# Optimization experiments

Hardware: AMD Instinct MI355X
Metric: run time of the kernel (lower is better)

Reference implementation:

```python
import jax, jax.numpy as jnp
import numpy as np

B, N, HID, NHEADS, VOCAB = 8, 2048, 768, 4, 15
ALPHA = 0.2  # LeakyReLU negative slope
NEG = -9e15  # matches -9000000000000000.0 mask constant


def setup_inputs() -> dict:
    key = jax.random.key(0)
    ks = jax.random.split(key, 7)
    node_feats = jax.random.randint(ks[0], (B, N), 0, VOCAB, dtype=jnp.int32)
    adjs = jax.random.randint(ks[1], (B, N, N), 0, 2, dtype=jnp.int32)
    embed_table = jax.random.normal(ks[2], (VOCAB, HID), dtype=jnp.float32)
    W_heads = jax.random.normal(ks[3], (NHEADS, HID, HID), dtype=jnp.float32) * 0.05
    a_heads = jax.random.normal(ks[4], (NHEADS, 2 * HID, 1), dtype=jnp.float32) * 0.05
    W_out = jax.random.normal(ks[5], (NHEADS * HID, HID), dtype=jnp.float32) * 0.05
    a_out = jax.random.normal(ks[6], (2 * HID, 1), dtype=jnp.float32) * 0.05
    return {"node_feats": node_feats, "adjs": adjs, "embed_table": embed_table,
            "W_heads": W_heads, "a_heads": a_heads, "W_out": W_out, "a_out": a_out}


def gat_layer(h, adj, W, a, concat):
    # h: (B,N,Fin), adj: (B,N,N), W: (Fin,Fout), a: (2*Fout,1)
    Fout = W.shape[1]
    Wh = jnp.matmul(h, W)                      # (B,N,Fout)
    Wh1 = jnp.matmul(Wh, a[:Fout])             # (B,N,1)
    Wh2 = jnp.matmul(Wh, a[Fout:])             # (B,N,1)
    e = Wh1 + jnp.swapaxes(Wh2, 1, 2)          # (B,N,N)
    e = jax.nn.leaky_relu(e, negative_slope=ALPHA)
    e = jnp.where(adj > 0, e, NEG)
    att = jax.nn.softmax(e, axis=-1)           # (B,N,N)
    h_prime = jnp.matmul(att, Wh)              # (B,N,Fout)
    return jax.nn.elu(h_prime) if concat else h_prime


def reference(node_feats, adjs, embed_table, W_heads, a_heads, W_out, a_out):
    x = embed_table[node_feats]                # (B,N,HID)  (shape_enc treated as identity)
    # multi-head GAT, heads vmapped then concatenated along feature dim
    heads = jax.vmap(lambda W, a: gat_layer(x, adjs, W, a, concat=True))(W_heads, a_heads)
    x = jnp.concatenate(jnp.moveaxis(heads, 0, -2).reshape(B, N, 1, NHEADS * HID).squeeze(2)[None], axis=0)[0] if False else jnp.transpose(heads, (1, 2, 0, 3)).reshape(B, N, NHEADS * HID)
    x = jax.nn.elu(gat_layer(x, adjs, W_out, a_out, concat=False))  # (B,N,HID)
    # pooling_forward with all-ones mask -> masked mean over node dim
    sum_emb = jnp.sum(x, axis=1)               # (B,HID)
    denom = jnp.maximum(jnp.full_like(sum_emb, float(N)), 1e-9)
    return sum_emb / denom                     # (B,HID)
```

## Files before the change

### kernel.cpp

```cpp
#include <hip/hip_runtime.h>
#include <math.h>

#define BB 8
#define NN 2048
#define HID 768
#define NHEADS 4
#define VOCAB 15
#define ALPHA 0.2f
#define NEGV -9e15f
#define MTOT (BB * NN)

using short4v = __attribute__((ext_vector_type(4))) short;
using short8v = __attribute__((ext_vector_type(8))) short;
using f32x4 = __attribute__((ext_vector_type(4))) float;

__device__ __forceinline__ short f2bf(float f) {
  union { float f; unsigned u; } x;
  x.f = f;
  unsigned r = x.u + 0x7fffu + ((x.u >> 16) & 1u);
  return (short)(r >> 16);
}

__device__ __forceinline__ void cp16(const void* g, void* l) {
  __builtin_amdgcn_global_load_lds(
      (const __attribute__((address_space(1))) unsigned int*)g,
      (__attribute__((address_space(3))) unsigned int*)l, 16, 0, 0);
}

__device__ __forceinline__ unsigned long long nibcompress(unsigned long long x) {
  x = (x | (x >> 4)) & 0x00FF00FF00FF00FFull;
  x = (x | (x >> 8)) & 0x0000FFFF0000FFFFull;
  x = (x | (x >> 16)) & 0x00000000FFFFFFFFull;
  return x;
}

#define MEMFENCE asm volatile("" ::: "memory")
#define SBAR()                         \
  do {                                 \
    MEMFENCE;                          \
    __builtin_amdgcn_s_barrier();      \
    MEMFENCE;                          \
  } while (0)

#define PACK_B 32768
#define ZERO_B 308
#define NFM_B 64
#define TRAN_B 2304
#define TW_B 192
__global__ __launch_bounds__(256) void setup_kernel(
    const int* __restrict__ adj, unsigned long long* __restrict__ packed,
    float* __restrict__ zbase, const int* __restrict__ nf,
    unsigned long long* __restrict__ nfm, const float* __restrict__ W_out,
    short* __restrict__ Wt_o, const float* __restrict__ table,
    const float* __restrict__ W_heads, float* __restrict__ TWp) {
  const int bid = blockIdx.x;
  const int tid = threadIdx.x;
  if (bid < PACK_B) {
    __shared__ unsigned long long nibq[32];
    long base = (long)bid * 1024;
    int4 a = *(const int4*)(adj + base + tid * 4);
    unsigned nib = (a.x > 0 ? 1u : 0u) | (a.y > 0 ? 2u : 0u) |
                   (a.z > 0 ? 4u : 0u) | (a.w > 0 ? 8u : 0u);
    ((unsigned char*)nibq)[tid] = (unsigned char)nib;
    __syncthreads();
    if (tid < 16) {
      unsigned long long lo = nibcompress(nibq[2 * tid]);
      unsigned long long hi = nibcompress(nibq[2 * tid + 1]);
      packed[(base >> 6) + tid] = lo | (hi << 32);
    }
  } else if (bid < PACK_B + ZERO_B) {
    zbase[(bid - PACK_B) * 256 + tid] = 0.f;
  } else if (bid < PACK_B + ZERO_B + NFM_B) {
    int r = bid - PACK_B - ZERO_B;
    int b = r >> 3, c = r & 7;
    int w = tid >> 6;
    int j = c * 256 + tid;
    int nfv = nf[b * NN + j];
#pragma unroll
    for (int v = 0; v < VOCAB; ++v) {
      unsigned long long m = __ballot(nfv == v);
      if ((tid & 63) == 0) nfm[((long)b * VOCAB + v) * 32 + c * 4 + w] = m;
    }
  } else if (bid < PACK_B + ZERO_B + NFM_B + TRAN_B) {
    __shared__ float t[32][33];
    int r2 = bid - PACK_B - ZERO_B - NFM_B;
    const int K = NHEADS * HID, N = HID;
    int k0 = (r2 % 96) * 32, n0 = (r2 / 96) * 32;
    int tx = tid & 31, ty = tid >> 5;
#pragma unroll
    for (int i = 0; i < 32; i += 8)
      t[ty + i][tx] = W_out[(long)(k0 + ty + i) * N + n0 + tx];
    __syncthreads();
#pragma unroll
    for (int i = 0; i < 32; i += 8)
      Wt_o[(long)(n0 + ty + i) * K + k0 + tx] = f2bf(t[tx][ty + i]);
  } else {
    __shared__ float tbl[VOCAB][48];
    int r3 = bid - PACK_B - ZERO_B - NFM_B - TRAN_B;
    const int cx = r3 % 12, ky = r3 / 12;
    const int c = cx * 256 + tid;
    const int h = (cx * 256) / HID;
    const int n = c - h * HID;
    const int k0 = ky * 48;
    for (int idx = tid; idx < VOCAB * 48; idx += 256)
      tbl[idx / 48][idx % 48] = table[(idx / 48) * HID + k0 + idx % 48];
    __syncthreads();
    float acc[VOCAB];
#pragma unroll
    for (int v = 0; v < VOCAB; ++v) acc[v] = 0.f;
    const float* wp = W_heads + (long)h * HID * HID + (long)k0 * HID + n;
#pragma unroll 8
    for (int kk = 0; kk < 48; ++kk) {
      float w = wp[(long)kk * HID];
#pragma unroll
      for (int v = 0; v < VOCAB; ++v) acc[v] = fmaf(tbl[v][kk], w, acc[v]);
    }
#pragma unroll
    for (int v = 0; v < VOCAB; ++v)
      TWp[((long)ky * VOCAB + v) * (NHEADS * HID) + c] = acc[v];
  }
}

__global__ __launch_bounds__(256) void tw_finish_kernel(
    const float* __restrict__ TWp, float* __restrict__ TW,
    const float* __restrict__ a_heads, float* __restrict__ TW1,
    float* __restrict__ TW2) {
  const int tid = threadIdx.x;
  const int c = blockIdx.x * 256 + tid;
  const int h = (blockIdx.x * 256) / HID;
  const int n = c - h * HID;
  const float a1 = a_heads[h * 2 * HID + n];
  const float a2 = a_heads[h * 2 * HID + HID + n];
  const int lane = tid & 63;
  const int wv = tid >> 6;
  __shared__ float red[4][2 * VOCAB];

  float s1[VOCAB], s2[VOCAB];
#pragma unroll
  for (int v = 0; v < VOCAB; ++v) {
    float s = 0.f;
#pragma unroll
    for (int ky = 0; ky < 16; ++ky)
      s += TWp[((long)ky * VOCAB + v) * (NHEADS * HID) + c];
    TW[v * (NHEADS * HID) + c] = s;
    s1[v] = s * a1;
    s2[v] = s * a2;
  }
#pragma unroll
  for (int off = 1; off < 64; off <<= 1)
#pragma unroll
    for (int v = 0; v < VOCAB; ++v) {
      s1[v] += __shfl_xor(s1[v], off);
      s2[v] += __shfl_xor(s2[v], off);
    }
  if (lane == 0) {
#pragma unroll
    for (int v = 0; v < VOCAB; ++v) {
      red[wv][v] = s1[v];
      red[wv][VOCAB + v] = s2[v];
    }
  }
  __syncthreads();
  if (tid < 2 * VOCAB) {
    float s = red[0][tid] + red[1][tid] + red[2][tid] + red[3][tid];
    float* dst = (tid < VOCAB) ? (TW1 + h * VOCAB + tid)
                               : (TW2 + h * VOCAB + tid - VOCAB);
    atomicAdd(dst, s);
  }
}

__global__ __launch_bounds__(256) void p16_kernel(
    const int* __restrict__ nf, const unsigned* __restrict__ padj32,
    const unsigned* __restrict__ nfm32, const float* __restrict__ TW1,
    const float* __restrict__ TW2, float* __restrict__ P16) {
  const int t = threadIdx.x;
  const int wv = t >> 6;
  const int lane = t & 63;
  const int rowm = blockIdx.x * 4 + wv;
  const int b = rowm >> 11;
  __shared__ float cnts[4][16];

  unsigned a = padj32[(long)rowm * 64 + lane];
  const unsigned* nb = nfm32 + (long)b * VOCAB * 64 + lane;
  int cnt[VOCAB];
#pragma unroll
  for (int v = 0; v < VOCAB; ++v) cnt[v] = __popc(a & nb[v * 64]);
#pragma unroll
  for (int off = 1; off < 64; off <<= 1)
#pragma unroll
    for (int v = 0; v < VOCAB; ++v) cnt[v] += __shfl_xor(cnt[v], off);
  int cntsum = 0;
#pragma unroll
  for (int v = 0; v < VOCAB; ++v) cntsum += cnt[v];
  const bool use_full = (cntsum == 0);
  if (use_full) {
#pragma unroll
    for (int v = 0; v < VOCAB; ++v) cnt[v] = __popc(nb[v * 64]);
#pragma unroll
    for (int off = 1; off < 64; off <<= 1)
#pragma unroll
      for (int v = 0; v < VOCAB; ++v) cnt[v] += __shfl_xor(cnt[v], off);
  }
  if (lane < 16) cnts[wv][lane] = (lane < VOCAB) ? (float)cnt[lane] : 0.f;
  __syncthreads();

  const int h = lane >> 4;
  const int v = lane & 15;
  const int nfi = nf[b * NN + (rowm & 2047)];
  float cvf = cnts[wv][v];
  bool valid = (v < VOCAB) && (cvf > 0.f);
  float logit = 0.f;
  if (!use_full) {
    float s = TW1[h * VOCAB + nfi] + ((v < VOCAB) ? TW2[h * VOCAB + v] : 0.f);
    logit = s > 0.f ? s : ALPHA * s;
  }
  float mv = valid ? logit : -INFINITY;
#pragma unroll
  for (int off = 1; off < 16; off <<= 1) mv = fmaxf(mv, __shfl_xor(mv, off));
  float pv = valid ? cvf * __expf(logit - mv) : 0.f;
  float sum = pv;
#pragma unroll
  for (int off = 1; off < 16; off <<= 1) sum += __shfl_xor(sum, off);
  if (v < VOCAB) P16[((long)h * 16384 + rowm) * 16 + v] = pv / sum;
}

__global__ __launch_bounds__(256) void hcat_expand(
    const float* __restrict__ TW, const float* __restrict__ P16,
    short* __restrict__ hcat) {
  __shared__ float twl[VOCAB * 128];
  __shared__ float pl[128 * 16];
  const int c0 = blockIdx.x * 128;
  const int r0 = blockIdx.y * 128;
  const int h = c0 / HID;
  const int t = threadIdx.x;
  for (int idx = t; idx < VOCAB * 128; idx += 256)
    twl[idx] = TW[(idx / 128) * (NHEADS * HID) + c0 + (idx & 127)];
  for (int idx = t; idx < 128 * 16; idx += 256)
    pl[idx] = P16[((long)h * 16384 + r0 + (idx >> 4)) * 16 + (idx & 15)];
  __syncthreads();
  const int clb = (t & 31) * 4;
  const int rlb = (t >> 5) * 16;
#pragma unroll 4
  for (int rr = 0; rr < 16; ++rr) {
    int rl = rlb + rr;
    short4v o;
#pragma unroll
    for (int cc = 0; cc < 4; ++cc) {
      float s = 0.f;
#pragma unroll
      for (int vv = 0; vv < VOCAB; ++vv)
        s = fmaf(pl[rl * 16 + vv], twl[vv * 128 + clb + cc], s);
      s = s > 0.f ? s : (__expf(s) - 1.f);
      o[cc] = f2bf(s);
    }
    *(short4v*)(hcat + (long)(r0 + rl) * (NHEADS * HID) + c0 + clb) = o;
  }
}

template <int MODE>
__global__ __launch_bounds__(512, 2) void mfma_gemm(
    const short* __restrict__ A, const short* __restrict__ B,
    int K, int lda, int ldb, long sA, long sB,
    float* __restrict__ Cf, short* __restrict__ Ct,
    const float* __restrict__ a_vec, float* __restrict__ Wh1g,
    float* __restrict__ Wh2g) {
  __shared__ short lds[2][2][16384];

  const int gx = gridDim.x, gy = gridDim.y;
  int linb = blockIdx.x + gx * (blockIdx.y + gy * blockIdx.z);
  const int per = (gx * gy * gridDim.z) >> 3;
  int work = (linb & 7) * per + (linb >> 3);
  const int bx = work % gx;
  int tmpw = work / gx;
  const int by = tmpw % gy;
  const int z = tmpw / gy;

  A += (long)z * sA;
  B += (long)z * sB;

  const int tid = threadIdx.x;
  const int m0 = by * 256;
  const int n0 = bx * 256;
  const int lane = tid & 63;
  const int wid = tid >> 6;
  const int wr = wid >> 2;
  const int wc = wid & 3;
  const int l15 = lane & 15;
  const int quad = lane >> 4;
  const int NT = K >> 6;

  const int cbase = (quad ^ (l15 & 7)) << 3;

  auto stageA = [&](int kt, int h) {
    const short* src = A + (long)(m0 + h * 128) * lda + kt * 64;
    short* dst = &lds[kt & 1][0][h * 8192];
#pragma unroll
    for (int it = 0; it < 2; ++it) {
      int r = it * 64 + (tid >> 3);
      int s = tid & 7;
      cp16(src + (long)r * lda + ((s ^ (r & 7)) << 3),
           dst + (it * 512 + tid) * 8);
    }
  };
  auto stageB = [&](int kt, int h) {
    const short* src = B + (long)(n0 + h * 128) * ldb + kt * 64;
    short* dst = &lds[kt & 1][1][h * 8192];
#pragma unroll
    for (int it = 0; it < 2; ++it) {
      int r = it * 64 + (tid >> 3);
      int s = tid & 7;
      cp16(src + (long)r * ldb + ((s ^ (r & 7)) << 3),
           dst + (it * 512 + tid) * 8);
    }
  };

  f32x4 acc[8][4];
#pragma unroll
  for (int i = 0; i < 8; ++i)
#pragma unroll
    for (int j = 0; j < 4; ++j) acc[i][j] = (f32x4){0.f, 0.f, 0.f, 0.f};

  stageA(0, 0); stageA(0, 1);
  stageB(0, 0); stageB(0, 1);
  stageA(1, 0); stageA(1, 1);
  asm volatile("s_waitcnt vmcnt(4)" ::: "memory");
  SBAR();

#pragma unroll 1
  for (int t = 0; t < NT; ++t) {
    const int p = t & 1;
    const short* Ab = &lds[p][0][0];
    const short* Bb = &lds[p][1][0];
    short8v a[4][2], b0[2][2], b1[2][2];

    if (t + 1 < NT) { stageB(t + 1, 0); stageB(t + 1, 1); }
#pragma unroll
    for (int ii = 0; ii < 4; ++ii) {
      int ro = (wr * 128 + ii * 16 + l15) * 64;
      a[ii][0] = *(const short8v*)(Ab + ro + cbase);
      a[ii][1] = *(const short8v*)(Ab + ro + (cbase ^ 32));
    }
#pragma unroll
    for (int jj = 0; jj < 2; ++jj) {
      int ro = (wc * 64 + jj * 16 + l15) * 64;
      b0[jj][0] = *(const short8v*)(Bb + ro + cbase);
      b0[jj][1] = *(const short8v*)(Bb + ro + (cbase ^ 32));
    }
    SBAR();
    asm volatile("s_waitcnt lgkmcnt(0)" ::: "memory");
    __builtin_amdgcn_sched_barrier(0);
    __builtin_amdgcn_s_setprio(1);
#pragma unroll
    for (int ii = 0; ii < 4; ++ii)
#pragma unroll
      for (int jj = 0; jj < 2; ++jj) {
        acc[ii][jj] = __builtin_amdgcn_mfma_f32_16x16x32_bf16(
            a[ii][0], b0[jj][0], acc[ii][jj], 0, 0, 0);
        acc[ii][jj] = __builtin_amdgcn_mfma_f32_16x16x32_bf16(
            a[ii][1], b0[jj][1], acc[ii][jj], 0, 0, 0);
      }
    __builtin_amdgcn_sched_barrier(0);
    __builtin_amdgcn_s_setprio(0);
    SBAR();

#pragma unroll
    for (int jj = 0; jj < 2; ++jj) {
      int ro = (wc * 64 + 32 + jj * 16 + l15) * 64;
      b1[jj][0] = *(const short8v*)(Bb + ro + cbase);
      b1[jj][1] = *(const short8v*)(Bb + ro + (cbase ^ 32));
    }
    SBAR();
    asm volatile("s_waitcnt lgkmcnt(0)" ::: "memory");
    __builtin_amdgcn_sched_barrier(0);
    __builtin_amdgcn_s_setprio(1);
#pragma unroll
    for (int ii = 0; ii < 4; ++ii)
#pragma unroll
      for (int jj = 0; jj < 2; ++jj) {
        acc[ii][2 + jj] = __builtin_amdgcn_mfma_f32_16x16x32_bf16(
            a[ii][0], b1[jj][0], acc[ii][2 + jj], 0, 0, 0);
        acc[ii][2 + jj] = __builtin_amdgcn_mfma_f32_16x16x32_bf16(
            a[ii][1], b1[jj][1], acc[ii][2 + jj], 0, 0, 0);
      }
    __builtin_amdgcn_sched_barrier(0);
    __builtin_amdgcn_s_setprio(0);
    SBAR();

#pragma unroll
    for (int ii = 0; ii < 4; ++ii) {
      int ro = (wr * 128 + 64 + ii * 16 + l15) * 64;
      a[ii][0] = *(const short8v*)(Ab + ro + cbase);
      a[ii][1] = *(const short8v*)(Ab + ro + (cbase ^ 32));
    }
    SBAR();
    asm volatile("s_waitcnt lgkmcnt(0)" ::: "memory");
    __builtin_amdgcn_sched_barrier(0);
    __builtin_amdgcn_s_setprio(1);
#pragma unroll
    for (int ii = 0; ii < 4; ++ii)
#pragma unroll
      for (int jj = 0; jj < 2; ++jj) {
        acc[4 + ii][2 + jj] = __builtin_amdgcn_mfma_f32_16x16x32_bf16(
            a[ii][0], b1[jj][0], acc[4 + ii][2 + jj], 0, 0, 0);
        acc[4 + ii][2 + jj] = __builtin_amdgcn_mfma_f32_16x16x32_bf16(
            a[ii][1], b1[jj][1], acc[4 + ii][2 + jj], 0, 0, 0);
      }
    __builtin_amdgcn_sched_barrier(0);
    __builtin_amdgcn_s_setprio(0);
    SBAR();

    if (t + 2 < NT) { stageA(t + 2, 0); stageA(t + 2, 1); }
    __builtin_amdgcn_s_setprio(1);
#pragma unroll
    for (int ii = 0; ii < 4; ++ii)
#pragma unroll
      for (int jj = 0; jj < 2; ++jj) {
        acc[4 + ii][jj] = __builtin_amdgcn_mfma_f32_16x16x32_bf16(
            a[ii][0], b0[jj][0], acc[4 + ii][jj], 0, 0, 0);
        acc[4 + ii][jj] = __builtin_amdgcn_mfma_f32_16x16x32_bf16(
            a[ii][1], b0[jj][1], acc[4 + ii][jj], 0, 0, 0);
      }
    __builtin_amdgcn_sched_barrier(0);
    __builtin_amdgcn_s_setprio(0);
    if (t + 2 < NT) {
      asm volatile("s_waitcnt vmcnt(4)" ::: "memory");
    } else if (t + 1 < NT) {
      asm volatile("s_waitcnt vmcnt(0)" ::: "memory");
    }
    SBAR();
  }

  if constexpr (MODE == 3) {
#pragma unroll
    for (int nj = 0; nj < 4; ++nj) {
      int col = n0 + wc * 64 + nj * 16 + l15;
      float s = 0.f;
#pragma unroll
      for (int mi = 0; mi < 8; ++mi)
#pragma unroll
        for (int reg = 0; reg < 4; ++reg) {
          float v = acc[mi][nj][reg];
          s += v > 0.f ? v : (__expf(v) - 1.f);
        }
      s += __shfl_xor(s, 16);
      s += __shfl_xor(s, 32);
      if (quad == 0) atomicAdd(Cf + (long)z * HID + col, s * (1.0f / NN));
    }
  } else {
    float a1v[4], a2v[4];
#pragma unroll
    for (int nj = 0; nj < 4; ++nj) {
      int colh = n0 + wc * 64 + nj * 16 + l15;
      a1v[nj] = a_vec[colh];
      a2v[nj] = a_vec[HID + colh];
    }
#pragma unroll
    for (int mi = 0; mi < 8; ++mi) {
      int rb = m0 + wr * 128 + mi * 16 + quad * 4;
#pragma unroll
      for (int reg = 0; reg < 4; ++reg) {
        float s1 = 0.f, s2 = 0.f;
#pragma unroll
        for (int nj = 0; nj < 4; ++nj) {
          s1 = fmaf(acc[mi][nj][reg], a1v[nj], s1);
          s2 = fmaf(acc[mi][nj][reg], a2v[nj], s2);
        }
#pragma unroll
        for (int off = 1; off < 16; off <<= 1) {
          s1 += __shfl_xor(s1, off);
          s2 += __shfl_xor(s2, off);
        }
        if (l15 == 0) {
          atomicAdd(Wh1g + rb + reg, s1);
          atomicAdd(Wh2g + rb + reg, s2);
        }
      }
    }
    const int bb = m0 >> 11;
    const int ml0 = (m0 & 2047) + wr * 128;
#pragma unroll
    for (int mi = 0; mi < 8; ++mi) {
#pragma unroll
      for (int nj = 0; nj < 4; ++nj) {
        int colh = n0 + wc * 64 + nj * 16 + l15;
        short4v pk;
#pragma unroll
        for (int reg = 0; reg < 4; ++reg) pk[reg] = f2bf(acc[mi][nj][reg]);
        *(short4v*)(Ct + ((long)bb * HID + colh) * NN + ml0 + mi * 16 +
                    quad * 4) = pk;
      }
    }
  }
}

__global__ __launch_bounds__(256) void attn_softmax_kernel(
    const float* __restrict__ Wh1, const float* __restrict__ Wh2,
    const unsigned long long* __restrict__ packed, short* __restrict__ att,
    float* __restrict__ zA, int zn) {
  int row = blockIdx.x;
  if (row < zn) zA[row * 256 + threadIdx.x] = 0.f;
  int b = row >> 11;
  const unsigned char* bits = (const unsigned char*)(packed + (long)row * 32);
  const float* wh2b = Wh2 + b * NN;
  const int t = threadIdx.x;
  const int lane = t & 63;
  const int wv = t >> 6;

  unsigned m8 = bits[t];
  float wh1 = Wh1[row];
  float4 wa = ((const float4*)(wh2b + t * 8))[0];
  float4 wb = ((const float4*)(wh2b + t * 8))[1];
  float v[8] = {wa.x, wa.y, wa.z, wa.w, wb.x, wb.y, wb.z, wb.w};

  float lmax = -INFINITY;
#pragma unroll
  for (int k = 0; k < 8; ++k) {
    float s = wh1 + v[k];
    s = s > 0.f ? s : ALPHA * s;
    s = ((m8 >> k) & 1u) ? s : NEGV;
    v[k] = s;
    lmax = fmaxf(lmax, s);
  }

  __shared__ float redm[4], reds[4];
#pragma unroll
  for (int off = 32; off > 0; off >>= 1) lmax = fmaxf(lmax, __shfl_xor(lmax, off));
  if (lane == 0) redm[wv] = lmax;
  __syncthreads();
  float m = fmaxf(fmaxf(redm[0], redm[1]), fmaxf(redm[2], redm[3]));

  float lsum = 0.f;
#pragma unroll
  for (int k = 0; k < 8; ++k) {
    float p = __expf(v[k] - m);
    v[k] = p;
    lsum += p;
  }
#pragma unroll
  for (int off = 32; off > 0; off >>= 1) lsum += __shfl_xor(lsum, off);
  if (lane == 0) reds[wv] = lsum;
  __syncthreads();
  float inv = 1.f / (reds[0] + reds[1] + reds[2] + reds[3]);

  short8v o;
#pragma unroll
  for (int k = 0; k < 8; ++k) o[k] = f2bf(v[k] * inv);
  *(short8v*)(att + (long)row * NN + t * 8) = o;
}

extern "C" void kernel_launch(void* const* d_in, const int* in_sizes, int n_in,
                              void* d_out, int out_size, void* d_ws,
                              size_t ws_size, hipStream_t stream) {
  const int* node_feats = (const int*)d_in[0];
  const int* adjs = (const int*)d_in[1];
  const float* embed_table = (const float*)d_in[2];
  const float* W_heads = (const float*)d_in[3];
  const float* a_heads = (const float*)d_in[4];
  const float* W_out = (const float*)d_in[5];
  const float* a_out = (const float*)d_in[6];
  float* out = (float*)d_out;

  char* p = (char*)d_ws;
  short* Wt_o = (short*)p;  p += (size_t)HID * (NHEADS * HID) * 2;
  short* Wh_t = (short*)p;  p += (size_t)BB * HID * NN * 2;
  short* att2 = (short*)p;  p += (size_t)BB * NN * NN * 2;
  short* hcat = (short*)p;  p += (size_t)MTOT * NHEADS * HID * 2;
  unsigned long long* padj = (unsigned long long*)p;
  p += (size_t)BB * NN * NN / 8;
  float* P16 = (float*)p;   p += (size_t)NHEADS * 16384 * 16 * 4;
  float* Wh1 = (float*)p;   p += (size_t)16384 * 4;
  float* Wh2 = (float*)p;   p += (size_t)16384 * 4;
  float* TW1 = (float*)p;   p += (size_t)64 * 4;
  float* TW2 = (float*)p;   p += (size_t)64 * 4;
  p += (size_t)(ZERO_B * 256 - 2 * 16384 - 128) * 4;
  float* TWp = (float*)p;   p += (size_t)16 * VOCAB * NHEADS * HID * 4;
  float* TW = (float*)p;    p += (size_t)VOCAB * NHEADS * HID * 4;
  unsigned long long* nfm = (unsigned long long*)p;
  p += (size_t)BB * VOCAB * 32 * 8;
  if ((size_t)(p - (char*)d_ws) > ws_size) return;

  setup_kernel<<<PACK_B + ZERO_B + NFM_B + TRAN_B + TW_B, 256, 0, stream>>>(
      adjs, padj, Wh1, node_feats, nfm, W_out, Wt_o, embed_table, W_heads,
      TWp);

  tw_finish_kernel<<<12, 256, 0, stream>>>(TWp, TW, a_heads, TW1, TW2);
  p16_kernel<<<16384 / 4, 256, 0, stream>>>(
      node_feats, (const unsigned*)padj, (const unsigned*)nfm, TW1, TW2, P16);
  hcat_expand<<<dim3(24, 128), 256, 0, stream>>>(TW, P16, hcat);

  mfma_gemm<0><<<dim3(HID / 256, MTOT / 256, 1), 512, 0, stream>>>(
      hcat, Wt_o, NHEADS * HID, NHEADS * HID, NHEADS * HID, 0, 0,
      nullptr, Wh_t, a_out, Wh1, Wh2);
  attn_softmax_kernel<<<MTOT, 256, 0, stream>>>(Wh1, Wh2, padj, att2, out, 24);
  mfma_gemm<3><<<dim3(HID / 256, NN / 256, BB), 512, 0, stream>>>(
      att2, Wh_t, NN, NN, NN, (long)NN * NN, (long)HID * NN,
      out, nullptr, nullptr, nullptr, nullptr);
}
```

Measured before the change: 439.8 us.

## Rework adjacency packing, hcat expand, GEMM A-load schedule and batched softmax rows

Several unrelated tweaks land together. Adjacency packing now has each thread read 16 ints, which cuts the block count by 4x and drops the nibble-compress shuffle. hcat_expand keeps TW columns in registers and reads P rows as float4 instead of staging both through LDS. The GEMM loads the upper-half A fragments ahead of time alongside the B1 fragments, which removes one barrier phase at the cost of more registers. MODE 0 remaps block order to column-major. The softmax kernel handles 8 rows per block and reuses the Wh2 loads, which trades parallelism for fewer blocks.

```diff
diff --git a/kernel.cpp b/kernel.cpp
--- a/kernel.cpp
+++ b/kernel.cpp
@@ -27,13 +27,6 @@
       (__attribute__((address_space(3))) unsigned int*)l, 16, 0, 0);
 }
 
-__device__ __forceinline__ unsigned long long nibcompress(unsigned long long x) {
-  x = (x | (x >> 4)) & 0x00FF00FF00FF00FFull;
-  x = (x | (x >> 8)) & 0x0000FFFF0000FFFFull;
-  x = (x | (x >> 16)) & 0x00000000FFFFFFFFull;
-  return x;
-}
-
 #define MEMFENCE asm volatile("" ::: "memory")
 #define SBAR()                         \
   do {                                 \
@@ -42,7 +35,7 @@
     MEMFENCE;                          \
   } while (0)
 
-#define PACK_B 32768
+#define PACK_B 8192
 #define ZERO_B 308
 #define NFM_B 64
 #define TRAN_B 2304
@@ -56,17 +49,26 @@
   const int bid = blockIdx.x;
   const int tid = threadIdx.x;
   if (bid < PACK_B) {
-    __shared__ unsigned long long nibq[32];
-    long base = (long)bid * 1024;
-    int4 a = *(const int4*)(adj + base + tid * 4);
-    unsigned nib = (a.x > 0 ? 1u : 0u) | (a.y > 0 ? 2u : 0u) |
-                   (a.z > 0 ? 4u : 0u) | (a.w > 0 ? 8u : 0u);
-    ((unsigned char*)nibq)[tid] = (unsigned char)nib;
+    __shared__ unsigned short us[256];
+    long base = (long)bid * 4096;
+    const int4* ap = (const int4*)(adj + base + tid * 16);
+    unsigned nib16 = 0;
+#pragma unroll
+    for (int k = 0; k < 4; ++k) {
+      int4 a = ap[k];
+      unsigned nib = (a.x > 0 ? 1u : 0u) | (a.y > 0 ? 2u : 0u) |
+                     (a.z > 0 ? 4u : 0u) | (a.w > 0 ? 8u : 0u);
+      nib16 |= nib << (4 * k);
+    }
+    us[tid] = (unsigned short)nib16;
     __syncthreads();
-    if (tid < 16) {
-      unsigned long long lo = nibcompress(nibq[2 * tid]);
-      unsigned long long hi = nibcompress(nibq[2 * tid + 1]);
-      packed[(base >> 6) + tid] = lo | (hi << 32);
+    if (tid < 64) {
+      unsigned long long w =
+          (unsigned long long)us[4 * tid] |
+          ((unsigned long long)us[4 * tid + 1] << 16) |
+          ((unsigned long long)us[4 * tid + 2] << 32) |
+          ((unsigned long long)us[4 * tid + 3] << 48);
+      packed[(base >> 6) + tid] = w;
     }
   } else if (bid < PACK_B + ZERO_B) {
     zbase[(bid - PACK_B) * 256 + tid] = 0.f;
@@ -227,29 +229,38 @@
 __global__ __launch_bounds__(256) void hcat_expand(
     const float* __restrict__ TW, const float* __restrict__ P16,
     short* __restrict__ hcat) {
-  __shared__ float twl[VOCAB * 128];
   __shared__ float pl[128 * 16];
   const int c0 = blockIdx.x * 128;
   const int r0 = blockIdx.y * 128;
   const int h = c0 / HID;
   const int t = threadIdx.x;
-  for (int idx = t; idx < VOCAB * 128; idx += 256)
-    twl[idx] = TW[(idx / 128) * (NHEADS * HID) + c0 + (idx & 127)];
   for (int idx = t; idx < 128 * 16; idx += 256)
     pl[idx] = P16[((long)h * 16384 + r0 + (idx >> 4)) * 16 + (idx & 15)];
-  __syncthreads();
   const int clb = (t & 31) * 4;
   const int rlb = (t >> 5) * 16;
+  float twc[VOCAB][4];
+#pragma unroll
+  for (int vv = 0; vv < VOCAB; ++vv) {
+    float4 q = *(const float4*)(TW + (long)vv * (NHEADS * HID) + c0 + clb);
+    twc[vv][0] = q.x; twc[vv][1] = q.y; twc[vv][2] = q.z; twc[vv][3] = q.w;
+  }
+  __syncthreads();
 #pragma unroll 4
   for (int rr = 0; rr < 16; ++rr) {
     int rl = rlb + rr;
+    const float* pr = pl + rl * 16;
+    float4 p0 = *(const float4*)(pr);
+    float4 p1 = *(const float4*)(pr + 4);
+    float4 p2 = *(const float4*)(pr + 8);
+    float4 p3 = *(const float4*)(pr + 12);
+    float pv[VOCAB] = {p0.x, p0.y, p0.z, p0.w, p1.x, p1.y, p1.z, p1.w,
+                       p2.x, p2.y, p2.z, p2.w, p3.x, p3.y, p3.z};
     short4v o;
 #pragma unroll
     for (int cc = 0; cc < 4; ++cc) {
       float s = 0.f;
 #pragma unroll
-      for (int vv = 0; vv < VOCAB; ++vv)
-        s = fmaf(pl[rl * 16 + vv], twl[vv * 128 + clb + cc], s);
+      for (int vv = 0; vv < VOCAB; ++vv) s = fmaf(pv[vv], twc[vv][cc], s);
       s = s > 0.f ? s : (__expf(s) - 1.f);
       o[cc] = f2bf(s);
     }
@@ -270,10 +281,17 @@
   int linb = blockIdx.x + gx * (blockIdx.y + gy * blockIdx.z);
   const int per = (gx * gy * gridDim.z) >> 3;
   int work = (linb & 7) * per + (linb >> 3);
-  const int bx = work % gx;
-  int tmpw = work / gx;
-  const int by = tmpw % gy;
-  const int z = tmpw / gy;
+  int bx, by, z;
+  if constexpr (MODE == 0) {
+    bx = work / gy;
+    by = work % gy;
+    z = 0;
+  } else {
+    bx = work % gx;
+    int tm = work / gx;
+    by = tm % gy;
+    z = tm / gy;
+  }
 
   A += (long)z * sA;
   B += (long)z * sB;
@@ -288,7 +306,6 @@
   const int l15 = lane & 15;
   const int quad = lane >> 4;
   const int NT = K >> 6;
-
   const int cbase = (quad ^ (l15 & 7)) << 3;
 
   auto stageA = [&](int kt, int h) {
@@ -331,14 +348,14 @@
     const int p = t & 1;
     const short* Ab = &lds[p][0][0];
     const short* Bb = &lds[p][1][0];
-    short8v a[4][2], b0[2][2], b1[2][2];
+    short8v alo[4][2], ahi[4][2], b0[2][2], b1[2][2];
 
     if (t + 1 < NT) { stageB(t + 1, 0); stageB(t + 1, 1); }
 #pragma unroll
     for (int ii = 0; ii < 4; ++ii) {
       int ro = (wr * 128 + ii * 16 + l15) * 64;
-      a[ii][0] = *(const short8v*)(Ab + ro + cbase);
-      a[ii][1] = *(const short8v*)(Ab + ro + (cbase ^ 32));
+      alo[ii][0] = *(const short8v*)(Ab + ro + cbase);
+      alo[ii][1] = *(const short8v*)(Ab + ro + (cbase ^ 32));
     }
 #pragma unroll
     for (int jj = 0; jj < 2; ++jj) {
@@ -355,9 +372,9 @@
 #pragma unroll
       for (int jj = 0; jj < 2; ++jj) {
         acc[ii][jj] = __builtin_amdgcn_mfma_f32_16x16x32_bf16(
-            a[ii][0], b0[jj][0], acc[ii][jj], 0, 0, 0);
+            alo[ii][0], b0[jj][0], acc[ii][jj], 0, 0, 0);
         acc[ii][jj] = __builtin_amdgcn_mfma_f32_16x16x32_bf16(
-            a[ii][1], b0[jj][1], acc[ii][jj], 0, 0, 0);
+            alo[ii][1], b0[jj][1], acc[ii][jj], 0, 0, 0);
       }
     __builtin_amdgcn_sched_barrier(0);
     __builtin_amdgcn_s_setprio(0);
@@ -369,6 +386,12 @@
       b1[jj][0] = *(const short8v*)(Bb + ro + cbase);
       b1[jj][1] = *(const short8v*)(Bb + ro + (cbase ^ 32));
     }
+#pragma unroll
+    for (int ii = 0; ii < 4; ++ii) {
+      int ro = (wr * 128 + 64 + ii * 16 + l15) * 64;
+      ahi[ii][0] = *(const short8v*)(Ab + ro + cbase);
+      ahi[ii][1] = *(const short8v*)(Ab + ro + (cbase ^ 32));
+    }
     SBAR();
     asm volatile("s_waitcnt lgkmcnt(0)" ::: "memory");
     __builtin_amdgcn_sched_barrier(0);
@@ -378,37 +401,23 @@
 #pragma unroll
       for (int jj = 0; jj < 2; ++jj) {
         acc[ii][2 + jj] = __builtin_amdgcn_mfma_f32_16x16x32_bf16(
-            a[ii][0], b1[jj][0], acc[ii][2 + jj], 0, 0, 0);
+            alo[ii][0], b1[jj][0], acc[ii][2 + jj], 0, 0, 0);
         acc[ii][2 + jj] = __builtin_amdgcn_mfma_f32_16x16x32_bf16(
-            a[ii][1], b1[jj][1], acc[ii][2 + jj], 0, 0, 0);
+            alo[ii][1], b1[jj][1], acc[ii][2 + jj], 0, 0, 0);
+      }
+#pragma unroll
+    for (int ii = 0; ii < 4; ++ii)
+#pragma unroll
+      for (int jj = 0; jj < 2; ++jj) {
+        acc[4 + ii][2 + jj] = __builtin_amdgcn_mfma_f32_16x16x32_bf16(
+            ahi[ii][0], b1[jj][0], acc[4 + ii][2 + jj], 0, 0, 0);
+        acc[4 + ii][2 + jj] = __builtin_amdgcn_mfma_f32_16x16x32_bf16(
+            ahi[ii][1], b1[jj][1], acc[4 + ii][2 + jj], 0, 0, 0);
       }
     __builtin_amdgcn_sched_barrier(0);
     __builtin_amdgcn_s_setprio(0);
     SBAR();
 
-#pragma unroll
-    for (int ii = 0; ii < 4; ++ii) {
-      int ro = (wr * 128 + 64 + ii * 16 + l15) * 64;
-      a[ii][0] = *(const short8v*)(Ab + ro + cbase);
-      a[ii][1] = *(const short8v*)(Ab + ro + (cbase ^ 32));
-    }
-    SBAR();
-    asm volatile("s_waitcnt lgkmcnt(0)" ::: "memory");
-    __builtin_amdgcn_sched_barrier(0);
-    __builtin_amdgcn_s_setprio(1);
-#pragma unroll
-    for (int ii = 0; ii < 4; ++ii)
-#pragma unroll
-      for (int jj = 0; jj < 2; ++jj) {
-        acc[4 + ii][2 + jj] = __builtin_amdgcn_mfma_f32_16x16x32_bf16(
-            a[ii][0], b1[jj][0], acc[4 + ii][2 + jj], 0, 0, 0);
-        acc[4 + ii][2 + jj] = __builtin_amdgcn_mfma_f32_16x16x32_bf16(
-            a[ii][1], b1[jj][1], acc[4 + ii][2 + jj], 0, 0, 0);
-      }
-    __builtin_amdgcn_sched_barrier(0);
-    __builtin_amdgcn_s_setprio(0);
-    SBAR();
-
     if (t + 2 < NT) { stageA(t + 2, 0); stageA(t + 2, 1); }
     __builtin_amdgcn_s_setprio(1);
 #pragma unroll
@@ -416,9 +425,9 @@
 #pragma unroll
       for (int jj = 0; jj < 2; ++jj) {
         acc[4 + ii][jj] = __builtin_amdgcn_mfma_f32_16x16x32_bf16(
-            a[ii][0], b0[jj][0], acc[4 + ii][jj], 0, 0, 0);
+            ahi[ii][0], b0[jj][0], acc[4 + ii][jj], 0, 0, 0);
         acc[4 + ii][jj] = __builtin_amdgcn_mfma_f32_16x16x32_bf16(
-            a[ii][1], b0[jj][1], acc[4 + ii][jj], 0, 0, 0);
+            ahi[ii][1], b0[jj][1], acc[4 + ii][jj], 0, 0, 0);
       }
     __builtin_amdgcn_sched_barrier(0);
     __builtin_amdgcn_s_setprio(0);
@@ -497,55 +506,60 @@
     const float* __restrict__ Wh1, const float* __restrict__ Wh2,
     const unsigned long long* __restrict__ packed, short* __restrict__ att,
     float* __restrict__ zA, int zn) {
-  int row = blockIdx.x;
-  if (row < zn) zA[row * 256 + threadIdx.x] = 0.f;
-  int b = row >> 11;
-  const unsigned char* bits = (const unsigned char*)(packed + (long)row * 32);
-  const float* wh2b = Wh2 + b * NN;
+  const int bid = blockIdx.x;
   const int t = threadIdx.x;
+  if (bid < zn) zA[bid * 256 + t] = 0.f;
+  const int b = bid >> 8;
+  const int row0 = bid * 8;
   const int lane = t & 63;
   const int wv = t >> 6;
-
-  unsigned m8 = bits[t];
-  float wh1 = Wh1[row];
+  const float* wh2b = Wh2 + b * NN;
+
   float4 wa = ((const float4*)(wh2b + t * 8))[0];
   float4 wb = ((const float4*)(wh2b + t * 8))[1];
-  float v[8] = {wa.x, wa.y, wa.z, wa.w, wb.x, wb.y, wb.z, wb.w};
-
-  float lmax = -INFINITY;
-#pragma unroll
-  for (int k = 0; k < 8; ++k) {
-    float s = wh1 + v[k];
-    s = s > 0.f ? s : ALPHA * s;
-    s = ((m8 >> k) & 1u) ? s : NEGV;
-    v[k] = s;
-    lmax = fmaxf(lmax, s);
-  }
+  float w[8] = {wa.x, wa.y, wa.z, wa.w, wb.x, wb.y, wb.z, wb.w};
 
   __shared__ float redm[4], reds[4];
-#pragma unroll
-  for (int off = 32; off > 0; off >>= 1) lmax = fmaxf(lmax, __shfl_xor(lmax, off));
-  if (lane == 0) redm[wv] = lmax;
-  __syncthreads();
-  float m = fmaxf(fmaxf(redm[0], redm[1]), fmaxf(redm[2], redm[3]));
-
-  float lsum = 0.f;
-#pragma unroll
-  for (int k = 0; k < 8; ++k) {
-    float p = __expf(v[k] - m);
-    v[k] = p;
-    lsum += p;
-  }
-#pragma unroll
-  for (int off = 32; off > 0; off >>= 1) lsum += __shfl_xor(lsum, off);
-  if (lane == 0) reds[wv] = lsum;
-  __syncthreads();
-  float inv = 1.f / (reds[0] + reds[1] + reds[2] + reds[3]);
-
-  short8v o;
-#pragma unroll
-  for (int k = 0; k < 8; ++k) o[k] = f2bf(v[k] * inv);
-  *(short8v*)(att + (long)row * NN + t * 8) = o;
+#pragma unroll 1
+  for (int r = 0; r < 8; ++r) {
+    const int row = row0 + r;
+    unsigned m8 = ((const unsigned char*)(packed + (long)row * 32))[t];
+    float wh1 = Wh1[row];
+    float v[8];
+    float lmax = -INFINITY;
+#pragma unroll
+    for (int k = 0; k < 8; ++k) {
+      float s = wh1 + w[k];
+      s = s > 0.f ? s : ALPHA * s;
+      s = ((m8 >> k) & 1u) ? s : NEGV;
+      v[k] = s;
+      lmax = fmaxf(lmax, s);
+    }
+#pragma unroll
+    for (int off = 32; off > 0; off >>= 1)
+      lmax = fmaxf(lmax, __shfl_xor(lmax, off));
+    if (lane == 0) redm[wv] = lmax;
+    __syncthreads();
+    float m = fmaxf(fmaxf(redm[0], redm[1]), fmaxf(redm[2], redm[3]));
+
+    float lsum = 0.f;
+#pragma unroll
+    for (int k = 0; k < 8; ++k) {
+      float p = __expf(v[k] - m);
+      v[k] = p;
+      lsum += p;
+    }
+#pragma unroll
+    for (int off = 32; off > 0; off >>= 1) lsum += __shfl_xor(lsum, off);
+    if (lane == 0) reds[wv] = lsum;
+    __syncthreads();
+    float inv = 1.f / (reds[0] + reds[1] + reds[2] + reds[3]);
+
+    short8v o;
+#pragma unroll
+    for (int k = 0; k < 8; ++k) o[k] = f2bf(v[k] * inv);
+    *(short8v*)(att + (long)row * NN + t * 8) = o;
+  }
 }
 
 extern "C" void kernel_launch(void* const* d_in, const int* in_sizes, int n_in,
@@ -591,7 +605,8 @@
   mfma_gemm<0><<<dim3(HID / 256, MTOT / 256, 1), 512, 0, stream>>>(
       hcat, Wt_o, NHEADS * HID, NHEADS * HID, NHEADS * HID, 0, 0,
       nullptr, Wh_t, a_out, Wh1, Wh2);
-  attn_softmax_kernel<<<MTOT, 256, 0, stream>>>(Wh1, Wh2, padj, att2, out, 24);
+  attn_softmax_kernel<<<MTOT / 8, 256, 0, stream>>>(Wh1, Wh2, padj, att2, out,
+                                                    24);
   mfma_gemm<3><<<dim3(HID / 256, NN / 256, BB), 512, 0, stream>>>(
       att2, Wh_t, NN, NN, NN, (long)NN * NN, (long)HID * NN,
       out, nullptr, nullptr, nullptr, nullptr);
```

After: 445.0 us. About the same (+1.2%).
